# Kernel optimization log

Hardware: AMD Instinct MI355X
Metric: run time of the kernel (lower is better)

The kernel has to match this reference:

```python
import jax, jax.numpy as jnp
import numpy as np

K = 1024       # num mixture components
D = 6          # state_dim (pos + vel)
B = 16384      # number of query points


def setup_inputs() -> dict:
    key = jax.random.key(0)
    k1, k2, k3, k4 = jax.random.split(key, 4)
    x = jax.random.normal(k1, (B, D), dtype=jnp.float32)
    means = jax.random.normal(k2, (K, D), dtype=jnp.float32)
    # SPD covariances: F @ F^T / D + 0.1 * I
    F = jax.random.normal(k3, (K, D, D), dtype=jnp.float32)
    covs = jnp.einsum('kij,klj->kil', F, F) / D + 0.1 * jnp.eye(D, dtype=jnp.float32)
    w = jax.random.uniform(k4, (K,), dtype=jnp.float32, minval=0.1, maxval=1.0)
    weights = w / jnp.sum(w)
    return {"x": x, "means": means, "covs": covs, "weights": weights}


def reference(x, means, covs, weights):
    """Batched GMM.log_pdf: for each point x_b, logsumexp_k [log w_k + log N(x_b; mu_k, Sigma_k)].
    Same math as the equinox module (Cholesky + triangular solve per component),
    vectorized over both components and query points.
    Returns log_pdf of shape [B]."""
    L = jnp.linalg.cholesky(covs)                      # [K, D, D]
    diff = x[:, None, :] - means[None, :, :]           # [B, K, D]
    # Solve L_k y = diff for all points at once: b has shape [K, D, B]
    b = jnp.transpose(diff, (1, 2, 0))                 # [K, D, B]
    y = jax.scipy.linalg.solve_triangular(L, b, lower=True)  # [K, D, B]
    quad = jnp.sum(y * y, axis=1)                      # [K, B]
    log_det = 2.0 * jnp.sum(jnp.log(jnp.diagonal(L, axis1=-2, axis2=-1)), axis=-1)  # [K]
    k_dim = means.shape[-1]
    log_prob = -0.5 * (k_dim * jnp.log(2.0 * jnp.pi) + log_det[:, None] + quad)      # [K, B]
    log_comp = jnp.log(weights)[:, None] + log_prob    # [K, B]
    return jax.scipy.special.logsumexp(log_comp, axis=0)  # [B]
```

## Files before the change

### kernel.cpp

```cpp
#include <hip/hip_runtime.h>
#include <hip/hip_bf16.h>
#include <math.h>

#define KCOMP 1024
#define DDIM  6
#define BPTS  16384

#define PTS    64
#define NWAVE  16
#define NTPW   4

typedef __attribute__((ext_vector_type(8))) short bf16x8;
typedef __attribute__((ext_vector_type(4))) float f32x4;

__device__ __forceinline__ unsigned short f32_to_bf16(float f) {
    unsigned int u = __float_as_uint(f);
    u += 0x7fffu + ((u >> 16) & 1u);
    return (unsigned short)(u >> 16);
}
__device__ __forceinline__ float bf16_to_f32(unsigned short h) {
    return __uint_as_float(((unsigned int)h) << 16);
}

__global__ __launch_bounds__(64, 1) void gmm_precompute(
        const float* __restrict__ means,
        const float* __restrict__ covs,
        const float* __restrict__ weights,
        unsigned short* __restrict__ Wh,
        unsigned short* __restrict__ Wl) {
    int k = blockIdx.x * 64 + threadIdx.x;
    if (k >= KCOMP) return;

    float A[6][6];
    const float* C = covs + k * 36;
    #pragma unroll
    for (int i = 0; i < 6; i++)
        #pragma unroll
        for (int j = 0; j < 6; j++)
            A[i][j] = C[i * 6 + j];

    float dprod = 1.0f;
    #pragma unroll
    for (int j = 0; j < 6; j++) {
        float d = A[j][j];
        #pragma unroll
        for (int t = 0; t < 6; t++) if (t < j) d -= A[j][t] * A[j][t];
        float ljj = __builtin_amdgcn_sqrtf(d);
        dprod *= ljj;
        A[j][j] = ljj;
        float inv = __builtin_amdgcn_rcpf(ljj);
        #pragma unroll
        for (int i = 0; i < 6; i++) {
            if (i > j) {
                float s = A[i][j];
                #pragma unroll
                for (int t = 0; t < 6; t++) if (t < j) s -= A[i][t] * A[j][t];
                A[i][j] = s * inv;
            }
        }
    }
    float logdet2 = 2.0f * __builtin_amdgcn_logf(dprod);

    float Li[6][6];
    #pragma unroll
    for (int j = 0; j < 6; j++) {
        Li[j][j] = __builtin_amdgcn_rcpf(A[j][j]);
        #pragma unroll
        for (int i = 0; i < 6; i++) {
            if (i > j) {
                float s = 0.0f;
                #pragma unroll
                for (int t = 0; t < 6; t++) if (t >= j && t < i) s += A[i][t] * Li[t][j];
                Li[i][j] = -s * __builtin_amdgcn_rcpf(A[i][i]);
            }
        }
    }

    #pragma unroll
    for (int i = 0; i < 6; i++) {
        #pragma unroll
        for (int j = 0; j < 6; j++) {
            if (j >= i) {
                float s = 0.0f;
                int lo = (i > j) ? i : j;
                #pragma unroll
                for (int t = 0; t < 6; t++) if (t >= lo) s += Li[t][i] * Li[t][j];
                A[i][j] = s;
                A[j][i] = s;
            }
        }
    }

    const float* mu = means + k * 6;
    float m[6];
    #pragma unroll
    for (int i = 0; i < 6; i++) m[i] = mu[i];

    float b[6];
    float muPmu = 0.0f;
    #pragma unroll
    for (int i = 0; i < 6; i++) {
        float s = 0.0f;
        #pragma unroll
        for (int j = 0; j < 6; j++) s += A[i][j] * m[j];
        b[i] = s;
        muPmu += s * m[i];
    }

    const float LOG2_2PI = 2.6514961294723187f;
    const float LOG2E    = 1.4426950408889634f;
    float c2 = __builtin_amdgcn_logf(weights[k])
             - 0.5f * (6.0f * LOG2_2PI + logdet2)
             - 0.5f * LOG2E * muPmu;

    float wv[32];
    int t = 0;
    #pragma unroll
    for (int i = 0; i < 6; i++)
        #pragma unroll
        for (int j = 0; j < 6; j++)
            if (j >= i) wv[t++] = LOG2E * ((i == j) ? -0.5f * A[i][j] : -A[i][j]);
    #pragma unroll
    for (int i = 0; i < 6; i++) wv[t++] = LOG2E * b[i];
    wv[27] = c2;
    wv[28] = 0.0f; wv[29] = 0.0f; wv[30] = 0.0f; wv[31] = 0.0f;

    int ntile = k >> 4, n15 = k & 15;
    #pragma unroll
    for (int kk = 0; kk < 32; kk++) {
        float v = wv[kk];
        unsigned short h = f32_to_bf16(v);
        unsigned short l = f32_to_bf16(v - bf16_to_f32(h));
        int idx = ((ntile * 64) + ((kk >> 3) << 4) + n15) * 8 + (kk & 7);
        Wh[idx] = h;
        Wl[idx] = l;
    }
}

__global__ __launch_bounds__(1024, 4) void gmm_main(
        const float* __restrict__ x,
        const unsigned short* __restrict__ Wh,
        const unsigned short* __restrict__ Wl,
        float* __restrict__ out) {
    const int tid  = threadIdx.x;
    const int lane = tid & 63;
    const int w    = __builtin_amdgcn_readfirstlane(tid >> 6);
    const int quad = lane >> 4;
    const int m15  = lane & 15;
    const int pbase = blockIdx.x * PTS;

    __shared__ bf16x8 fragA[8][64];
    __shared__ float  partial[NWAVE][PTS];

    if (w < 8) {
        const int pt    = w & 3;
        const int split = w >> 2;
        float v[6];
        const float* xp = x + (pbase + pt * 16 + m15) * 6;
        #pragma unroll
        for (int i = 0; i < 6; i++) v[i] = xp[i];

        float f[8];
        if (quad == 0) {
            f[0]=v[0]*v[0]; f[1]=v[0]*v[1]; f[2]=v[0]*v[2]; f[3]=v[0]*v[3];
            f[4]=v[0]*v[4]; f[5]=v[0]*v[5]; f[6]=v[1]*v[1]; f[7]=v[1]*v[2];
        } else if (quad == 1) {
            f[0]=v[1]*v[3]; f[1]=v[1]*v[4]; f[2]=v[1]*v[5]; f[3]=v[2]*v[2];
            f[4]=v[2]*v[3]; f[5]=v[2]*v[4]; f[6]=v[2]*v[5]; f[7]=v[3]*v[3];
        } else if (quad == 2) {
            f[0]=v[3]*v[4]; f[1]=v[3]*v[5]; f[2]=v[4]*v[4]; f[3]=v[4]*v[5];
            f[4]=v[5]*v[5]; f[5]=v[0];      f[6]=v[1];      f[7]=v[2];
        } else {
            f[0]=v[3]; f[1]=v[4]; f[2]=v[5]; f[3]=1.0f;
            f[4]=0.0f; f[5]=0.0f; f[6]=0.0f; f[7]=0.0f;
        }

        bf16x8 frag;
        #pragma unroll
        for (int j = 0; j < 8; j++) {
            unsigned short h = f32_to_bf16(f[j]);
            frag[j] = (split == 0) ? (short)h
                                   : (short)f32_to_bf16(f[j] - bf16_to_f32(h));
        }
        fragA[w][lane] = frag;
    }
    __syncthreads();

    bf16x8 Ah[4], Al[4];
    #pragma unroll
    for (int pt = 0; pt < 4; pt++) {
        Ah[pt] = fragA[pt][lane];
        Al[pt] = fragA[4 + pt][lane];
    }

    const bf16x8* WhF = (const bf16x8*)Wh + (w * NTPW) * 64;
    const bf16x8* WlF = (const bf16x8*)Wl + (w * NTPW) * 64;

    float esum[4][4];
    #pragma unroll
    for (int pt = 0; pt < 4; pt++)
        #pragma unroll
        for (int r = 0; r < 4; r++) esum[pt][r] = 0.0f;

    #pragma unroll
    for (int t = 0; t < NTPW; t++) {
        bf16x8 bh = WhF[t * 64 + lane];
        bf16x8 bl = WlF[t * 64 + lane];
        #pragma unroll
        for (int pt = 0; pt < 4; pt++) {
            f32x4 c = {0.0f, 0.0f, 0.0f, 0.0f};
            c = __builtin_amdgcn_mfma_f32_16x16x32_bf16(Ah[pt], bh, c, 0, 0, 0);
            c = __builtin_amdgcn_mfma_f32_16x16x32_bf16(Al[pt], bh, c, 0, 0, 0);
            c = __builtin_amdgcn_mfma_f32_16x16x32_bf16(Ah[pt], bl, c, 0, 0, 0);
            #pragma unroll
            for (int r = 0; r < 4; r++)
                esum[pt][r] += __builtin_amdgcn_exp2f(c[r]);
        }
    }

    #pragma unroll
    for (int pt = 0; pt < 4; pt++) {
        #pragma unroll
        for (int r = 0; r < 4; r++) {
            float v = esum[pt][r];
            v += __shfl_xor(v, 1);
            v += __shfl_xor(v, 2);
            v += __shfl_xor(v, 4);
            v += __shfl_xor(v, 8);
            esum[pt][r] = v;
        }
    }

    if (m15 == 0) {
        #pragma unroll
        for (int pt = 0; pt < 4; pt++)
            #pragma unroll
            for (int r = 0; r < 4; r++)
                partial[w][pt * 16 + quad * 4 + r] = esum[pt][r];
    }
    __syncthreads();

    if (tid < PTS) {
        float S = 0.0f;
        #pragma unroll
        for (int c = 0; c < NWAVE; c++) S += partial[c][tid];
        const float LN2 = 0.6931471805599453f;
        out[pbase + tid] = LN2 * __builtin_amdgcn_logf(S);
    }
}

extern "C" void kernel_launch(void* const* d_in, const int* in_sizes, int n_in,
                              void* d_out, int out_size, void* d_ws, size_t ws_size,
                              hipStream_t stream) {
    const float* x       = (const float*)d_in[0];
    const float* means   = (const float*)d_in[1];
    const float* covs    = (const float*)d_in[2];
    const float* weights = (const float*)d_in[3];
    float* out = (float*)d_out;

    unsigned short* Wh = (unsigned short*)d_ws;
    unsigned short* Wl = Wh + 32768;

    gmm_precompute<<<KCOMP / 64, 64, 0, stream>>>(means, covs, weights, Wh, Wl);
    gmm_main<<<BPTS / PTS, 1024, 0, stream>>>(x, Wh, Wl, out);
}
```

Baseline: 66.96 us.

## Fuse GMM parameter precompute into main kernel, staging weights in LDS

Removes the separate precompute kernel and has every block recompute all component Cholesky factors, precision terms and bf16 hi/lo splits, writing them into shared memory instead of a global workspace. This removes one kernel launch and the global write/read round trip of the packed weights. In exchange every block repeats the full per-component precompute and loads all covariances, and the 128KB LDS staging limits occupancy to one block per CU.

```diff
diff --git a/kernel.cpp b/kernel.cpp
--- a/kernel.cpp
+++ b/kernel.cpp
@@ -22,125 +22,11 @@
     return __uint_as_float(((unsigned int)h) << 16);
 }
 
-__global__ __launch_bounds__(64, 1) void gmm_precompute(
+__global__ __launch_bounds__(1024, 4) void gmm_fused(
+        const float* __restrict__ x,
         const float* __restrict__ means,
         const float* __restrict__ covs,
         const float* __restrict__ weights,
-        unsigned short* __restrict__ Wh,
-        unsigned short* __restrict__ Wl) {
-    int k = blockIdx.x * 64 + threadIdx.x;
-    if (k >= KCOMP) return;
-
-    float A[6][6];
-    const float* C = covs + k * 36;
-    #pragma unroll
-    for (int i = 0; i < 6; i++)
-        #pragma unroll
-        for (int j = 0; j < 6; j++)
-            A[i][j] = C[i * 6 + j];
-
-    float dprod = 1.0f;
-    #pragma unroll
-    for (int j = 0; j < 6; j++) {
-        float d = A[j][j];
-        #pragma unroll
-        for (int t = 0; t < 6; t++) if (t < j) d -= A[j][t] * A[j][t];
-        float ljj = __builtin_amdgcn_sqrtf(d);
-        dprod *= ljj;
-        A[j][j] = ljj;
-        float inv = __builtin_amdgcn_rcpf(ljj);
-        #pragma unroll
-        for (int i = 0; i < 6; i++) {
-            if (i > j) {
-                float s = A[i][j];
-                #pragma unroll
-                for (int t = 0; t < 6; t++) if (t < j) s -= A[i][t] * A[j][t];
-                A[i][j] = s * inv;
-            }
-        }
-    }
-    float logdet2 = 2.0f * __builtin_amdgcn_logf(dprod);
-
-    float Li[6][6];
-    #pragma unroll
-    for (int j = 0; j < 6; j++) {
-        Li[j][j] = __builtin_amdgcn_rcpf(A[j][j]);
-        #pragma unroll
-        for (int i = 0; i < 6; i++) {
-            if (i > j) {
-                float s = 0.0f;
-                #pragma unroll
-                for (int t = 0; t < 6; t++) if (t >= j && t < i) s += A[i][t] * Li[t][j];
-                Li[i][j] = -s * __builtin_amdgcn_rcpf(A[i][i]);
-            }
-        }
-    }
-
-    #pragma unroll
-    for (int i = 0; i < 6; i++) {
-        #pragma unroll
-        for (int j = 0; j < 6; j++) {
-            if (j >= i) {
-                float s = 0.0f;
-                int lo = (i > j) ? i : j;
-                #pragma unroll
-                for (int t = 0; t < 6; t++) if (t >= lo) s += Li[t][i] * Li[t][j];
-                A[i][j] = s;
-                A[j][i] = s;
-            }
-        }
-    }
-
-    const float* mu = means + k * 6;
-    float m[6];
-    #pragma unroll
-    for (int i = 0; i < 6; i++) m[i] = mu[i];
-
-    float b[6];
-    float muPmu = 0.0f;
-    #pragma unroll
-    for (int i = 0; i < 6; i++) {
-        float s = 0.0f;
-        #pragma unroll
-        for (int j = 0; j < 6; j++) s += A[i][j] * m[j];
-        b[i] = s;
-        muPmu += s * m[i];
-    }
-
-    const float LOG2_2PI = 2.6514961294723187f;
-    const float LOG2E    = 1.4426950408889634f;
-    float c2 = __builtin_amdgcn_logf(weights[k])
-             - 0.5f * (6.0f * LOG2_2PI + logdet2)
-             - 0.5f * LOG2E * muPmu;
-
-    float wv[32];
-    int t = 0;
-    #pragma unroll
-    for (int i = 0; i < 6; i++)
-        #pragma unroll
-        for (int j = 0; j < 6; j++)
-            if (j >= i) wv[t++] = LOG2E * ((i == j) ? -0.5f * A[i][j] : -A[i][j]);
-    #pragma unroll
-    for (int i = 0; i < 6; i++) wv[t++] = LOG2E * b[i];
-    wv[27] = c2;
-    wv[28] = 0.0f; wv[29] = 0.0f; wv[30] = 0.0f; wv[31] = 0.0f;
-
-    int ntile = k >> 4, n15 = k & 15;
-    #pragma unroll
-    for (int kk = 0; kk < 32; kk++) {
-        float v = wv[kk];
-        unsigned short h = f32_to_bf16(v);
-        unsigned short l = f32_to_bf16(v - bf16_to_f32(h));
-        int idx = ((ntile * 64) + ((kk >> 3) << 4) + n15) * 8 + (kk & 7);
-        Wh[idx] = h;
-        Wl[idx] = l;
-    }
-}
-
-__global__ __launch_bounds__(1024, 4) void gmm_main(
-        const float* __restrict__ x,
-        const unsigned short* __restrict__ Wh,
-        const unsigned short* __restrict__ Wl,
         float* __restrict__ out) {
     const int tid  = threadIdx.x;
     const int lane = tid & 63;
@@ -149,6 +35,8 @@
     const int m15  = lane & 15;
     const int pbase = blockIdx.x * PTS;
 
+    __shared__ short  WH[NWAVE * NTPW * 64 * 8];
+    __shared__ short  WL[NWAVE * NTPW * 64 * 8];
     __shared__ bf16x8 fragA[8][64];
     __shared__ float  partial[NWAVE][PTS];
 
@@ -184,6 +72,123 @@
         }
         fragA[w][lane] = frag;
     }
+
+    {
+        const int k = w * 64 + lane;
+
+        float A[6][6];
+        const float* C = covs + k * 36;
+        #pragma unroll
+        for (int i = 0; i < 6; i++)
+            #pragma unroll
+            for (int j = 0; j < 6; j++)
+                A[i][j] = C[i * 6 + j];
+
+        float dprod = 1.0f;
+        #pragma unroll
+        for (int j = 0; j < 6; j++) {
+            float d = A[j][j];
+            #pragma unroll
+            for (int t = 0; t < 6; t++) if (t < j) d -= A[j][t] * A[j][t];
+            float ljj = __builtin_amdgcn_sqrtf(d);
+            dprod *= ljj;
+            A[j][j] = ljj;
+            float inv = __builtin_amdgcn_rcpf(ljj);
+            #pragma unroll
+            for (int i = 0; i < 6; i++) {
+                if (i > j) {
+                    float s = A[i][j];
+                    #pragma unroll
+                    for (int t = 0; t < 6; t++) if (t < j) s -= A[i][t] * A[j][t];
+                    A[i][j] = s * inv;
+                }
+            }
+        }
+        float logdet2 = 2.0f * __builtin_amdgcn_logf(dprod);
+
+        float Li[6][6];
+        #pragma unroll
+        for (int j = 0; j < 6; j++) {
+            Li[j][j] = __builtin_amdgcn_rcpf(A[j][j]);
+            #pragma unroll
+            for (int i = 0; i < 6; i++) {
+                if (i > j) {
+                    float s = 0.0f;
+                    #pragma unroll
+                    for (int t = 0; t < 6; t++) if (t >= j && t < i) s += A[i][t] * Li[t][j];
+                    Li[i][j] = -s * __builtin_amdgcn_rcpf(A[i][i]);
+                }
+            }
+        }
+
+        #pragma unroll
+        for (int i = 0; i < 6; i++) {
+            #pragma unroll
+            for (int j = 0; j < 6; j++) {
+                if (j >= i) {
+                    float s = 0.0f;
+                    int lo = (i > j) ? i : j;
+                    #pragma unroll
+                    for (int t = 0; t < 6; t++) if (t >= lo) s += Li[t][i] * Li[t][j];
+                    A[i][j] = s;
+                    A[j][i] = s;
+                }
+            }
+        }
+
+        const float* mu = means + k * 6;
+        float m[6];
+        #pragma unroll
+        for (int i = 0; i < 6; i++) m[i] = mu[i];
+
+        float b[6];
+        float muPmu = 0.0f;
+        #pragma unroll
+        for (int i = 0; i < 6; i++) {
+            float s = 0.0f;
+            #pragma unroll
+            for (int j = 0; j < 6; j++) s += A[i][j] * m[j];
+            b[i] = s;
+            muPmu += s * m[i];
+        }
+
+        const float LOG2_2PI = 2.6514961294723187f;
+        const float LOG2E    = 1.4426950408889634f;
+        float c2 = __builtin_amdgcn_logf(weights[k])
+                 - 0.5f * (6.0f * LOG2_2PI + logdet2)
+                 - 0.5f * LOG2E * muPmu;
+
+        float wv[32];
+        int t = 0;
+        #pragma unroll
+        for (int i = 0; i < 6; i++)
+            #pragma unroll
+            for (int j = 0; j < 6; j++)
+                if (j >= i) wv[t++] = LOG2E * ((i == j) ? -0.5f * A[i][j] : -A[i][j]);
+        #pragma unroll
+        for (int i = 0; i < 6; i++) wv[t++] = LOG2E * b[i];
+        wv[27] = c2;
+        wv[28] = 0.0f; wv[29] = 0.0f; wv[30] = 0.0f; wv[31] = 0.0f;
+
+        const int tt   = lane >> 4;
+        const int base = (w * 4 + tt) * 64 + (lane & 15);
+        bf16x8* wh8 = (bf16x8*)WH;
+        bf16x8* wl8 = (bf16x8*)WL;
+        #pragma unroll
+        for (int kq = 0; kq < 4; kq++) {
+            bf16x8 ph, pl;
+            #pragma unroll
+            for (int j = 0; j < 8; j++) {
+                float v = wv[kq * 8 + j];
+                unsigned short h = f32_to_bf16(v);
+                ph[j] = (short)h;
+                pl[j] = (short)f32_to_bf16(v - bf16_to_f32(h));
+            }
+            wh8[base + kq * 16] = ph;
+            wl8[base + kq * 16] = pl;
+        }
+    }
+
     __syncthreads();
 
     bf16x8 Ah[4], Al[4];
@@ -193,8 +198,8 @@
         Al[pt] = fragA[4 + pt][lane];
     }
 
-    const bf16x8* WhF = (const bf16x8*)Wh + (w * NTPW) * 64;
-    const bf16x8* WlF = (const bf16x8*)Wl + (w * NTPW) * 64;
+    const bf16x8* wh8 = (const bf16x8*)WH + (w * NTPW) * 64;
+    const bf16x8* wl8 = (const bf16x8*)WL + (w * NTPW) * 64;
 
     float esum[4][4];
     #pragma unroll
@@ -204,8 +209,8 @@
 
     #pragma unroll
     for (int t = 0; t < NTPW; t++) {
-        bf16x8 bh = WhF[t * 64 + lane];
-        bf16x8 bl = WlF[t * 64 + lane];
+        bf16x8 bh = wh8[t * 64 + lane];
+        bf16x8 bl = wl8[t * 64 + lane];
         #pragma unroll
         for (int pt = 0; pt < 4; pt++) {
             f32x4 c = {0.0f, 0.0f, 0.0f, 0.0f};
@@ -257,10 +262,7 @@
     const float* covs    = (const float*)d_in[2];
     const float* weights = (const float*)d_in[3];
     float* out = (float*)d_out;
-
-    unsigned short* Wh = (unsigned short*)d_ws;
-    unsigned short* Wl = Wh + 32768;
-
-    gmm_precompute<<<KCOMP / 64, 64, 0, stream>>>(means, covs, weights, Wh, Wl);
-    gmm_main<<<BPTS / PTS, 1024, 0, stream>>>(x, Wh, Wl, out);
-}
+    (void)d_ws; (void)ws_size;
+
+    gmm_fused<<<BPTS / PTS, 1024, 0, stream>>>(x, means, covs, weights, out);
+}
```

Measured after the change: 68.52 us. +2.3%, slower.
